# Performance work log

Hardware: AMD Instinct MI355X
Metric: run time of the kernel (lower is better)

The kernel has to match this reference:

```python
import jax, jax.numpy as jnp
import numpy as np

N, E, B = 128000, 512000, 128

def _conv1d(x, w, b):
    # x: [B,C,L], w: [O,I,K] (torch layout) -> valid conv, stride 1
    y = jax.lax.conv_general_dilated(x, w, (1,), 'VALID',
                                     dimension_numbers=('NCH', 'OIH', 'NCH'))
    return y + b[None, :, None]

def setup_inputs():
    key = jax.random.key(0)
    ks = jax.random.split(key, 22)
    def u(k, shape, fan_in):
        bound = 1.0 / np.sqrt(fan_in)
        return jax.random.uniform(k, shape, jnp.float32, -bound, bound)
    x = jax.random.normal(ks[0], (N, 33), jnp.float32)
    edge_index = jax.random.randint(ks[1], (2, E), 0, N, dtype=jnp.int64)
    batch = (jnp.arange(N, dtype=jnp.int64) * B) // N  # sorted, every graph non-empty
    target = jax.random.normal(ks[2], (B, 26, 1000), jnp.float32)
    return {
        'x': x, 'edge_index': edge_index, 'batch': batch, 'target': target,
        'lin_w': u(ks[3], (256, 33), 33), 'lin_b': jnp.zeros((256,), jnp.float32),
        'conv1_w': u(ks[4], (64, 26, 3), 26 * 3), 'conv1_b': u(ks[5], (64,), 26 * 3),
        'conv2_w': u(ks[6], (256, 64, 3), 64 * 3), 'conv2_b': u(ks[7], (256,), 64 * 3),
        'conv3_w': u(ks[8], (1024, 256, 5), 256 * 5), 'conv3_b': u(ks[9], (1024,), 256 * 5),
        'fc_w': u(ks[10], (768, 1024), 1024), 'fc_b': u(ks[11], (768,), 1024),
        'm1_w': u(ks[12], (1024, 1024), 1024), 'm1_b': u(ks[13], (1024,), 1024),
        'm2_w': u(ks[14], (1024, 1024), 1024), 'm2_b': u(ks[15], (1024,), 1024),
        'm3_w': u(ks[16], (512, 1024), 1024), 'm3_b': u(ks[17], (512,), 1024),
        'm4_w': u(ks[18], (1, 512), 512), 'm4_b': u(ks[19], (1,), 512),
    }

def reference(x, edge_index, batch, target,
              lin_w, lin_b, conv1_w, conv1_b, conv2_w, conv2_b,
              conv3_w, conv3_b, fc_w, fc_b,
              m1_w, m1_b, m2_w, m2_b, m3_w, m3_b, m4_w, m4_b):
    # ---- drug branch: GCN-normalized message passing, sum-aggr, graph mean ----
    xw = x @ lin_w.T                                   # [N,256]
    row, col = edge_index[0], edge_index[1]            # source j, target i
    deg = jax.ops.segment_sum(jnp.ones((E,), x.dtype), col, num_segments=N)
    dis = jnp.where(deg > 0, deg ** -0.5, 0.0)
    norm = dis[row] * dis[col]                         # [E]
    agg = jax.ops.segment_sum(norm[:, None] * xw[row], col, num_segments=N)
    out = agg + lin_b                                  # [N,256]
    sums = jax.ops.segment_sum(out, batch, num_segments=B)
    cnt = jax.ops.segment_sum(jnp.ones((N,), x.dtype), batch, num_segments=B)
    drug = jnp.where(cnt[:, None] > 0, sums / cnt[:, None], 0.0)  # [B,256]
    # ---- target branch: CNN (dropout = identity in eval) ----
    h = jax.nn.relu(_conv1d(target, conv1_w, conv1_b))
    h = jax.nn.relu(_conv1d(h, conv2_w, conv2_b))
    h = jax.nn.relu(_conv1d(h, conv3_w, conv3_b))
    h = jnp.max(h, axis=2)                             # AdaptiveMaxPool1d(1) -> [B,1024]
    tgt = jax.nn.relu(h @ fc_w.T + fc_b)               # [B,768]
    # ---- head MLP ----
    z = jnp.concatenate([drug, tgt], axis=1)           # [B,1024]
    z = jax.nn.relu(z @ m1_w.T + m1_b)
    z = jax.nn.relu(z @ m2_w.T + m2_b)
    z = jax.nn.relu(z @ m3_w.T + m3_b)
    return z @ m4_w.T + m4_b                           # [B,1]
```

## Files before the change

kernel.cpp:

```cpp
#include <hip/hip_runtime.h>

typedef unsigned short u16;
typedef __attribute__((ext_vector_type(8))) short short8;
typedef __attribute__((ext_vector_type(4))) float f32x4;

#define NN 128000
#define EE 512000
#define GB 128

#define GLDS16(g, l)                                                     \
  __builtin_amdgcn_global_load_lds(                                      \
      (const __attribute__((address_space(1))) unsigned int*)(g),        \
      (__attribute__((address_space(3))) unsigned int*)(l), 16, 0, 0)

__device__ __forceinline__ float u2f(u16 u) {
  union { unsigned u32; float f; } v; v.u32 = ((unsigned)u) << 16; return v.f;
}
__device__ __forceinline__ u16 f2bf(float x) {
  union { float f; unsigned u; } v; v.f = x;
  unsigned r = v.u + 0x7FFF + ((v.u >> 16) & 1);
  return (u16)(r >> 16);
}

__global__ void k_transpose(const float* lin_w, const float* w1, const float* w2, const float* w3,
                            float* lin_wT, float* w1T, u16* w2t, u16* w3r) {
  int idx = blockIdx.x * 256 + threadIdx.x;
  if (idx < 8448) { int i = idx >> 8, o = idx & 255; lin_wT[idx] = lin_w[o * 33 + i]; return; }
  idx -= 8448;
  if (idx < 4992) { int o = idx & 63, ck = idx >> 6; w1T[idx] = w1[o * 78 + ck]; return; }
  idx -= 4992;
  if (idx < 49152) {
    int c = idx & 63, o = (idx >> 6) & 255, k = idx >> 14;
    w2t[idx] = f2bf(w2[o * 192 + c * 3 + k]);
    return;
  }
  idx -= 49152;
  if (idx < 1310720) {
    int k    = idx >> 18;
    int r    = idx & 262143;
    int ot   = r >> 16;
    int wn   = (r >> 14) & 3;
    int j    = (r >> 12) & 3;
    int cb   = (r >> 9) & 7;
    int quad = (r >> 7) & 3;
    int l16  = (r >> 3) & 15;
    int i    = r & 7;
    int o = ot * 256 + wn * 64 + j * 16 + l16;
    int c = cb * 32 + quad * 8 + i;
    w3r[idx] = f2bf(w3[o * 1280 + c * 5 + k]);
  }
}

__global__ void k_deg_start(const int* ei, const int* batch, int* deg, int* start, int* hist) {
  __shared__ int lh[GB];
  int tid = threadIdx.x, blk = blockIdx.x;
  if (tid < GB) lh[tid] = 0;
  __syncthreads();
  int e0 = blk * 1024;
#pragma unroll
  for (int t = 0; t < 4; t++) {
    int e = e0 + t * 256 + tid;
    int col = ei[EE + e];
    atomicAdd(&deg[col], 1);
    atomicAdd(&lh[batch[col]], 1);
  }
  int i = blk * 256 + tid;
  int b = batch[i];
  if (i == 0) start[0] = 0;
  else if (b != batch[i - 1]) start[b] = i;
  if (i == NN - 1) start[GB] = NN;
  __syncthreads();
  if (tid < GB && lh[tid]) atomicAdd(&hist[tid * 16], lh[tid]);
}

__global__ void k_prefix(const int* hist, int* off, int* cursor) {
  __shared__ int h[GB];
  int tid = threadIdx.x;
  h[tid] = hist[tid * 16];
  __syncthreads();
  int s = 0;
  for (int j = 0; j < tid; j++) s += h[j];
  off[tid] = s;
  cursor[tid * 16] = s;
  if (tid == GB - 1) off[GB] = s + h[GB - 1];
}

__global__ void k_xw(const float* x, const float* lin_wT, const int* deg, u16* xw, float* dis) {
  __shared__ float xs[32][34];
  int tid = threadIdx.x, n0 = blockIdx.x * 32;
  int q = tid >> 6, lane = tid & 63;
  for (int n = q; n < 32; n += 4)
    if (lane < 33) xs[n][lane] = x[(n0 + n) * 33 + lane];
  float w[33];
#pragma unroll
  for (int i = 0; i < 33; i++) w[i] = lin_wT[i * 256 + tid];
  __syncthreads();
  for (int n = 0; n < 32; n++) {
    float acc = 0.f;
#pragma unroll
    for (int i = 0; i < 33; i++) acc += w[i] * xs[n][i];
    xw[(size_t)(n0 + n) * 256 + tid] = f2bf(acc);
  }
  if (tid < 32) { int d = deg[n0 + tid]; dis[n0 + tid] = d > 0 ? rsqrtf((float)d) : 0.f; }
}

__global__ void k_scatter(const int* ei, const int* batch, const float* dis,
                          int* cursor, uint2* bucket) {
  __shared__ int lh[GB];
  __shared__ int lbase[GB];
  int tid = threadIdx.x, blk = blockIdx.x;
  if (tid < GB) lh[tid] = 0;
  __syncthreads();
  int e0 = blk * 1024;
  int row[4], g[4], rk[4]; float nrm[4];
#pragma unroll
  for (int t = 0; t < 4; t++) {
    int e = e0 + t * 256 + tid;
    int r = ei[e], c = ei[EE + e];
    row[t] = r;
    g[t] = batch[c];
    nrm[t] = dis[r] * dis[c];
    rk[t] = atomicAdd(&lh[g[t]], 1);
  }
  __syncthreads();
  if (tid < GB && lh[tid]) lbase[tid] = atomicAdd(&cursor[tid * 16], lh[tid]);
  __syncthreads();
#pragma unroll
  for (int t = 0; t < 4; t++) {
    uint2 v; v.x = (unsigned)row[t]; v.y = __float_as_uint(nrm[t]);
    bucket[lbase[g[t]] + rk[t]] = v;
  }
}

__global__ void k_gather(const uint2* bucket, const int* off, const u16* xw, float* gsum) {
  __shared__ float red[4][256];
  int tid = threadIdx.x;
  int s = blockIdx.x, g = blockIdx.y;
  int lo = off[g], hi = off[g + 1];
  int cnt = hi - lo;
  int per = (cnt + 15) >> 4;
  int b0 = lo + s * per, b1 = min(b0 + per, hi);
  int lane = tid & 63, wid = tid >> 6;
  f32x4 acc = {0.f, 0.f, 0.f, 0.f};
  const u16* xbase = xw + lane * 4;
#pragma unroll 8
  for (int e = b0 + wid; e < b1; e += 4) {
    uint2 be = bucket[e];
    float nrm = __uint_as_float(be.y);
    ushort4 v = *(const ushort4*)(xbase + (size_t)be.x * 256);
    acc.x = fmaf(nrm, u2f(v.x), acc.x);
    acc.y = fmaf(nrm, u2f(v.y), acc.y);
    acc.z = fmaf(nrm, u2f(v.z), acc.z);
    acc.w = fmaf(nrm, u2f(v.w), acc.w);
  }
  *(f32x4*)&red[wid][lane * 4] = acc;
  __syncthreads();
  float v = red[0][tid] + red[1][tid] + red[2][tid] + red[3][tid];
  if (v != 0.f) atomicAdd(&gsum[tid * 128 + g], v);
}

__global__ void k_conv1(const float* target, const float* w1T, const float* b1, u16* h1T) {
  __shared__ float ts[26][132];
  __shared__ float wls[78 * 64];
  int tid = threadIdx.x, lt = blockIdx.x, bl = blockIdx.y;
  int l0 = lt * 128;
  int q = tid >> 6, lane = tid & 63;
  for (int c = q; c < 26; c += 4)
    for (int i = lane; i < 130; i += 64)
      ts[c][i] = target[(bl * 26 + c) * 1000 + min(l0 + i, 999)];
  for (int i = tid; i < 4992; i += 256) wls[i] = w1T[i];
  __syncthreads();
  int o = tid & 63, wid = tid >> 6;
  float w[78];
#pragma unroll
  for (int i = 0; i < 78; i++) w[i] = wls[i * 64 + o];
  float bias = b1[o];
  for (int t = 0; t < 32; t++) {
    int li = wid * 32 + t;
    float acc = bias;
#pragma unroll
    for (int c = 0; c < 26; c++)
#pragma unroll
      for (int k = 0; k < 3; k++) acc += ts[c][li + k] * w[c * 3 + k];
    int lg = l0 + li;
    if (lg < 998) h1T[((size_t)bl * 1000 + lg) * 64 + o] = f2bf(fmaxf(acc, 0.f));
  }
}

__global__ void k_conv2(const u16* h1T, const u16* w2t, const float* b2, u16* h2T) {
  __shared__ __align__(16) u16 als[132 * 32];
  __shared__ __align__(16) u16 bls[3 * 128 * 32];
  int tid = threadIdx.x;
  int lt = blockIdx.x, ot = blockIdx.y, bl = blockIdx.z;
  int l0 = lt * 128, o0 = ot * 128;
  int lane = tid & 63, wid = tid >> 6;
  int wm = wid >> 1, wn = wid & 1;
  int quad = lane >> 4, l16 = lane & 15;
  const f32x4 zero = {0.f, 0.f, 0.f, 0.f};
  f32x4 acc[4][4];
#pragma unroll
  for (int i = 0; i < 4; i++)
#pragma unroll
    for (int j = 0; j < 4; j++) acc[i][j] = zero;
  for (int cb = 0; cb < 2; cb++) {
    int c0 = cb * 32;
#pragma unroll
    for (int rr = 0; rr < 2; rr++) {
      int cid = rr * 256 + wid * 64 + lane;
      int row = cid >> 2, ch = (cid & 3) ^ (row & 3);
      GLDS16(h1T + ((size_t)bl * 1000 + min(l0 + row, 997)) * 64 + c0 + ch * 8,
             als + (rr * 256 + wid * 64) * 8);
    }
    if (wid == 0 && lane < 8) {
      int cid = 512 + lane;
      int row = cid >> 2, ch = (cid & 3) ^ (row & 3);
      GLDS16(h1T + ((size_t)bl * 1000 + min(l0 + row, 997)) * 64 + c0 + ch * 8, als + 512 * 8);
    }
#pragma unroll
    for (int rr = 0; rr < 6; rr++) {
      int cid = rr * 256 + wid * 64 + lane;
      int rko = cid >> 2, k = rko >> 7, o = rko & 127;
      int ch = (cid & 3) ^ (rko & 3);
      GLDS16(w2t + ((size_t)(k * 256 + o0 + o)) * 64 + c0 + ch * 8,
             bls + (rr * 256 + wid * 64) * 8);
    }
    __syncthreads();
#pragma unroll
    for (int k = 0; k < 3; k++) {
      short8 af[4], bfr[4];
#pragma unroll
      for (int i = 0; i < 4; i++) {
        int row = k + wm * 64 + i * 16 + l16;
        af[i] = *(const short8*)(als + row * 32 + ((quad ^ (row & 3)) * 8));
      }
#pragma unroll
      for (int j = 0; j < 4; j++) {
        int rowB = wn * 64 + j * 16 + l16;
        bfr[j] = *(const short8*)(bls + (k * 128 + rowB) * 32 + ((quad ^ (rowB & 3)) * 8));
      }
#pragma unroll
      for (int i = 0; i < 4; i++)
#pragma unroll
        for (int j = 0; j < 4; j++)
          acc[i][j] = __builtin_amdgcn_mfma_f32_16x16x32_bf16(af[i], bfr[j], acc[i][j], 0, 0, 0);
    }
    __syncthreads();
  }
#pragma unroll
  for (int j = 0; j < 4; j++) {
    int col = o0 + wn * 64 + j * 16 + l16;
    float bias = b2[col];
#pragma unroll
    for (int i = 0; i < 4; i++)
#pragma unroll
      for (int r = 0; r < 4; r++) {
        int lg = l0 + wm * 64 + i * 16 + quad * 4 + r;
        if (lg < 996)
          h2T[((size_t)bl * 996 + lg) * 256 + col] = f2bf(fmaxf(acc[i][j][r] + bias, 0.f));
      }
  }
}

__global__ void __launch_bounds__(256, 2)
k_conv3(const u16* h2T, const u16* w3r, const float* b3, float* pooledT) {
  __shared__ __align__(16) u16 als[136 * 128];
  __shared__ float mbuf[256];
  int bid = blockIdx.x;
  int xc = bid & 7, rr0 = bid >> 3;
  int ot = rr0 & 3, bl = xc * 16 + (rr0 >> 2);
  int o0 = ot * 256;
  int tid = threadIdx.x;
  int lane = tid & 63, wn = tid >> 6;
  int quad = lane >> 4, l16 = lane & 15;
  float omax[4];
#pragma unroll
  for (int j = 0; j < 4; j++) omax[j] = -3.0e38f;
  const f32x4 zero = {0.f, 0.f, 0.f, 0.f};
  const u16* wbase = w3r + ((size_t)(ot * 4 + wn)) * 16384 + lane * 8;
  for (int lt = 0; lt < 8; lt++) {
    int l0 = lt * 128;
    f32x4 acc[8][4];
#pragma unroll
    for (int i = 0; i < 8; i++)
#pragma unroll
      for (int j = 0; j < 4; j++) acc[i][j] = zero;
#pragma unroll 1
    for (int st = 0; st < 2; st++) {
#pragma unroll
      for (int rr = 0; rr < 8; rr++) {
        int cid = rr * 256 + tid;
        int row = cid >> 4, pp = cid & 15;
        int cc = (pp - row) & 15;
        GLDS16(h2T + ((size_t)bl * 996 + min(l0 + row, 995)) * 256 + st * 128 + cc * 8,
               als + (rr * 256 + wn * 64) * 8);
      }
      if (wn < 2) {
        int cid = 2048 + wn * 64 + lane;
        int row = cid >> 4, pp = cid & 15;
        int cc = (pp - row) & 15;
        GLDS16(h2T + ((size_t)bl * 996 + min(l0 + row, 995)) * 256 + st * 128 + cc * 8,
               als + (2048 + wn * 64) * 8);
      }
      __syncthreads();
#pragma unroll 1
      for (int cb = 0; cb < 4; cb++) {
#pragma unroll
        for (int k = 0; k < 5; k++) {
          short8 breg[4];
#pragma unroll
          for (int j = 0; j < 4; j++)
            breg[j] = *(const short8*)(wbase + (size_t)k * 262144 + (size_t)j * 4096 +
                                       (size_t)(st * 4 + cb) * 512);
#pragma unroll
          for (int i = 0; i < 8; i++) {
            int row = k + i * 16 + l16;
            int pp = (cb * 4 + quad + row) & 15;
            short8 af = *(const short8*)(als + row * 128 + pp * 8);
#pragma unroll
            for (int j = 0; j < 4; j++)
              acc[i][j] = __builtin_amdgcn_mfma_f32_16x16x32_bf16(af, breg[j], acc[i][j],
                                                                  0, 0, 0);
          }
        }
      }
      __syncthreads();
    }
#pragma unroll
    for (int i = 0; i < 8; i++) {
#pragma unroll
      for (int r = 0; r < 4; r++) {
        int lg = l0 + i * 16 + quad * 4 + r;
        if (lg < 992) {
#pragma unroll
          for (int j = 0; j < 4; j++) omax[j] = fmaxf(omax[j], acc[i][j][r]);
        }
      }
    }
  }
#pragma unroll
  for (int j = 0; j < 4; j++) {
    omax[j] = fmaxf(omax[j], __shfl_xor(omax[j], 16, 64));
    omax[j] = fmaxf(omax[j], __shfl_xor(omax[j], 32, 64));
  }
  if (quad == 0) {
#pragma unroll
    for (int j = 0; j < 4; j++) mbuf[wn * 64 + j * 16 + l16] = omax[j];
  }
  __syncthreads();
  {
    float v = mbuf[tid] + b3[o0 + tid];
    pooledT[(size_t)(o0 + tid) * 128 + bl] = fmaxf(v, 0.f);
  }
}

__global__ void k_z0(const float* gsum, const int* start, const float* lin_b, const float* tgtT,
                     float* z0T) {
  int idx = blockIdx.x * 256 + threadIdx.x;
  int r = idx >> 7, bb = idx & 127;
  float v;
  if (r < 256) {
    float c = (float)(start[bb + 1] - start[bb]);
    v = gsum[idx] / c + lin_b[r];
  } else {
    v = tgtT[(r - 256) * 128 + bb];
  }
  z0T[idx] = v;
}

__global__ void k_fc4(const float* zT, const float* W, const float* bias, float* outT,
                      int K, int O) {
  __shared__ float wls[4 * 1024];
  int tid = threadIdx.x;
  int o0 = blockIdx.x * 4;
  for (int idx = tid; idx < 4 * K; idx += 512) {
    int oo = idx / K, i = idx - oo * K;
    wls[oo * K + i] = W[(size_t)(o0 + oo) * K + i];
  }
  __syncthreads();
  int osub = tid >> 7, bb = tid & 127;
  int o = o0 + osub;
  float acc = 0.f;
  const float* wp = &wls[osub * K];
#pragma unroll 8
  for (int i = 0; i < K; i++) acc = fmaf(wp[i], zT[i * 128 + bb], acc);
  acc += bias[o];
  outT[(size_t)o * 128 + bb] = fmaxf(acc, 0.f);
}

__global__ void k_fc_final(const float* zT, const float* W, const float* bias, float* final_out,
                           int K) {
  __shared__ float wls[512];
  int tid = threadIdx.x;
  for (int i = tid; i < K; i += 256) wls[i] = W[i];
  __syncthreads();
  if (tid >= 128) return;
  int bb = tid;
  float acc = 0.f;
#pragma unroll 8
  for (int i = 0; i < K; i++) acc = fmaf(wls[i], zT[i * 128 + bb], acc);
  final_out[bb] = acc + bias[0];
}

extern "C" void kernel_launch(void* const* d_in, const int* in_sizes, int n_in,
                              void* d_out, int out_size, void* d_ws, size_t ws_size,
                              hipStream_t stream) {
  const float* x      = (const float*)d_in[0];
  const int*   ei     = (const int*)d_in[1];
  const int*   batch  = (const int*)d_in[2];
  const float* target = (const float*)d_in[3];
  const float* lin_w  = (const float*)d_in[4];
  const float* lin_b  = (const float*)d_in[5];
  const float* w1     = (const float*)d_in[6];
  const float* b1     = (const float*)d_in[7];
  const float* w2     = (const float*)d_in[8];
  const float* b2     = (const float*)d_in[9];
  const float* w3     = (const float*)d_in[10];
  const float* b3     = (const float*)d_in[11];
  const float* fcw    = (const float*)d_in[12];
  const float* fcb    = (const float*)d_in[13];
  const float* m1w = (const float*)d_in[14]; const float* m1b = (const float*)d_in[15];
  const float* m2w = (const float*)d_in[16]; const float* m2b = (const float*)d_in[17];
  const float* m3w = (const float*)d_in[18]; const float* m3b = (const float*)d_in[19];
  const float* m4w = (const float*)d_in[20]; const float* m4b = (const float*)d_in[21];

  char* ws = (char*)d_ws;
  size_t ofs = 0;
  auto alloc = [&](size_t bytes) -> void* {
    void* p = ws + ofs;
    ofs = (ofs + bytes + 255) & ~(size_t)255;
    return p;
  };
  int*   deg    = (int*)alloc((size_t)NN * 4);
  float* dis    = (float*)alloc((size_t)NN * 4);
  int*   start  = (int*)alloc((size_t)(GB + 1) * 4);
  int*   hist   = (int*)alloc((size_t)GB * 16 * 4);
  int*   off    = (int*)alloc((size_t)(GB + 1) * 4);
  int*   cursor = (int*)alloc((size_t)GB * 16 * 4);
  uint2* bucket = (uint2*)alloc((size_t)EE * 8);
  float* gsum   = (float*)alloc((size_t)256 * 128 * 4);
  float* lin_wT = (float*)alloc((size_t)33 * 256 * 4);
  float* w1T    = (float*)alloc((size_t)78 * 64 * 4);
  u16*   w2t    = (u16*)alloc((size_t)3 * 256 * 64 * 2);
  u16*   w3r    = (u16*)alloc((size_t)5 * 1024 * 256 * 2);
  float* pooledT= (float*)alloc((size_t)1024 * 128 * 4);
  float* tgtT   = (float*)alloc((size_t)768 * 128 * 4);
  float* z0T    = (float*)alloc((size_t)1024 * 128 * 4);
  float* z1T    = (float*)alloc((size_t)1024 * 128 * 4);
  float* z2T    = (float*)alloc((size_t)1024 * 128 * 4);
  float* z3T    = (float*)alloc((size_t)512 * 128 * 4);
  size_t F_end = ofs;

  u16* xw  = (u16*)(ws + F_end);
  u16* h1T = (u16*)(ws + F_end);
  u16* h2T = (u16*)(ws + F_end + (size_t)128 * 1000 * 64 * 2);

  hipMemsetAsync(deg, 0, (size_t)NN * 4, stream);
  hipMemsetAsync(hist, 0, (size_t)GB * 16 * 4, stream);
  hipMemsetAsync(gsum, 0, (size_t)256 * 128 * 4, stream);

  k_transpose<<<5365, 256, 0, stream>>>(lin_w, w1, w2, w3, lin_wT, w1T, w2t, w3r);
  k_deg_start<<<500, 256, 0, stream>>>(ei, batch, deg, start, hist);
  k_prefix<<<1, 128, 0, stream>>>(hist, off, cursor);
  k_xw<<<4000, 256, 0, stream>>>(x, lin_wT, deg, xw, dis);
  k_scatter<<<500, 256, 0, stream>>>(ei, batch, dis, cursor, bucket);
  k_gather<<<dim3(16, GB), 256, 0, stream>>>(bucket, off, xw, gsum);

  k_conv1<<<dim3(8, 128), 256, 0, stream>>>(target, w1T, b1, h1T);
  k_conv2<<<dim3(8, 2, 128), 256, 0, stream>>>(h1T, w2t, b2, h2T);
  k_conv3<<<512, 256, 0, stream>>>(h2T, w3r, b3, pooledT);

  k_fc4<<<192, 512, 0, stream>>>(pooledT, fcw, fcb, tgtT, 1024, 768);
  k_z0<<<512, 256, 0, stream>>>(gsum, start, lin_b, tgtT, z0T);
  k_fc4<<<256, 512, 0, stream>>>(z0T, m1w, m1b, z1T, 1024, 1024);
  k_fc4<<<256, 512, 0, stream>>>(z1T, m2w, m2b, z2T, 1024, 1024);
  k_fc4<<<128, 512, 0, stream>>>(z2T, m3w, m3b, z3T, 1024, 512);
  k_fc_final<<<1, 256, 0, stream>>>(z3T, m4w, m4b, (float*)d_out, 512);
}
```

Measured before the change: 841.3 us.

## Repack conv3 weights by step and double-buffer B-fragment loads in registers

Reorders the bf16 conv3 weight packing so each (st, cb, k) step's B fragments for a wave sit in one contiguous 32K-element slab. The conv3 inner loop is unrolled into explicit steps that prefetch the next step's weight fragments into a second register set while the current set feeds the MFMAs, wrapping back to step 0 across l-tiles. The aim is to hide global weight-load latency behind matrix math. It costs extra VGPRs under the two-blocks-per-CU launch bound, which may cause spills or lower occupancy.

Result: slower. 1.100 ms (+30.8%).

```diff
diff --git a/kernel.cpp b/kernel.cpp
--- a/kernel.cpp
+++ b/kernel.cpp
@@ -23,7 +23,7 @@
 }
 
 __global__ void k_transpose(const float* lin_w, const float* w1, const float* w2, const float* w3,
-                            float* lin_wT, float* w1T, u16* w2t, u16* w3r) {
+                            float* lin_wT, float* w1T, u16* w2t, u16* w3p) {
   int idx = blockIdx.x * 256 + threadIdx.x;
   if (idx < 8448) { int i = idx >> 8, o = idx & 255; lin_wT[idx] = lin_w[o * 33 + i]; return; }
   idx -= 8448;
@@ -36,18 +36,14 @@
   }
   idx -= 49152;
   if (idx < 1310720) {
-    int k    = idx >> 18;
-    int r    = idx & 262143;
-    int ot   = r >> 16;
-    int wn   = (r >> 14) & 3;
-    int j    = (r >> 12) & 3;
-    int cb   = (r >> 9) & 7;
-    int quad = (r >> 7) & 3;
-    int l16  = (r >> 3) & 15;
-    int i    = r & 7;
-    int o = ot * 256 + wn * 64 + j * 16 + l16;
-    int c = cb * 32 + quad * 8 + i;
-    w3r[idx] = f2bf(w3[o * 1280 + c * 5 + k]);
+    int stcbk = idx >> 15;
+    int fi    = (idx >> 9) & 63;
+    int r512  = idx & 511;
+    int quad  = r512 >> 7, l16 = (r512 >> 3) & 15, i = r512 & 7;
+    int stcb  = stcbk / 5, k = stcbk - stcb * 5;
+    int o = fi * 16 + l16;
+    int c = stcb * 32 + quad * 8 + i;
+    w3p[idx] = f2bf(w3[o * 1280 + c * 5 + k]);
   }
 }
 
@@ -261,8 +257,32 @@
   }
 }
 
+#define LOADB(dst, s)                                                          \
+  do {                                                                         \
+    const u16* p_ = wb + (size_t)(s) * 32768;                                  \
+    dst[0] = *(const short8*)(p_);                                             \
+    dst[1] = *(const short8*)(p_ + 512);                                       \
+    dst[2] = *(const short8*)(p_ + 1024);                                      \
+    dst[3] = *(const short8*)(p_ + 1536);                                      \
+  } while (0)
+
+#define STEP(CUR, NXT, KK, CBV, SNEXT)                                         \
+  do {                                                                         \
+    LOADB(NXT, SNEXT);                                                         \
+    _Pragma("unroll")                                                          \
+    for (int i = 0; i < 8; i++) {                                              \
+      int row = (KK) + i * 16 + l16;                                           \
+      int pp = ((CBV) * 4 + quad + row) & 15;                                  \
+      short8 af = *(const short8*)(als + row * 128 + pp * 8);                  \
+      acc[i][0] = __builtin_amdgcn_mfma_f32_16x16x32_bf16(af, CUR[0], acc[i][0], 0, 0, 0); \
+      acc[i][1] = __builtin_amdgcn_mfma_f32_16x16x32_bf16(af, CUR[1], acc[i][1], 0, 0, 0); \
+      acc[i][2] = __builtin_amdgcn_mfma_f32_16x16x32_bf16(af, CUR[2], acc[i][2], 0, 0, 0); \
+      acc[i][3] = __builtin_amdgcn_mfma_f32_16x16x32_bf16(af, CUR[3], acc[i][3], 0, 0, 0); \
+    }                                                                          \
+  } while (0)
+
 __global__ void __launch_bounds__(256, 2)
-k_conv3(const u16* h2T, const u16* w3r, const float* b3, float* pooledT) {
+k_conv3(const u16* h2T, const u16* w3p, const float* b3, float* pooledT) {
   __shared__ __align__(16) u16 als[136 * 128];
   __shared__ float mbuf[256];
   int bid = blockIdx.x;
@@ -276,7 +296,9 @@
 #pragma unroll
   for (int j = 0; j < 4; j++) omax[j] = -3.0e38f;
   const f32x4 zero = {0.f, 0.f, 0.f, 0.f};
-  const u16* wbase = w3r + ((size_t)(ot * 4 + wn)) * 16384 + lane * 8;
+  const u16* wb = w3p + (size_t)(ot * 16 + wn * 4) * 512 + lane * 8;
+  short8 bA[4], bB[4];
+  LOADB(bA, 0);
   for (int lt = 0; lt < 8; lt++) {
     int l0 = lt * 128;
     f32x4 acc[8][4];
@@ -303,25 +325,20 @@
       }
       __syncthreads();
 #pragma unroll 1
-      for (int cb = 0; cb < 4; cb++) {
-#pragma unroll
-        for (int k = 0; k < 5; k++) {
-          short8 breg[4];
-#pragma unroll
-          for (int j = 0; j < 4; j++)
-            breg[j] = *(const short8*)(wbase + (size_t)k * 262144 + (size_t)j * 4096 +
-                                       (size_t)(st * 4 + cb) * 512);
-#pragma unroll
-          for (int i = 0; i < 8; i++) {
-            int row = k + i * 16 + l16;
-            int pp = (cb * 4 + quad + row) & 15;
-            short8 af = *(const short8*)(als + row * 128 + pp * 8);
-#pragma unroll
-            for (int j = 0; j < 4; j++)
-              acc[i][j] = __builtin_amdgcn_mfma_f32_16x16x32_bf16(af, breg[j], acc[i][j],
-                                                                  0, 0, 0);
-          }
-        }
+      for (int cbp = 0; cbp < 2; cbp++) {
+        int cb0 = cbp * 2, cb1 = cb0 + 1;
+        int sb = st * 20 + cbp * 10;
+        int swrap = (sb == 30) ? 0 : sb + 10;
+        STEP(bA, bB, 0, cb0, sb + 1);
+        STEP(bB, bA, 1, cb0, sb + 2);
+        STEP(bA, bB, 2, cb0, sb + 3);
+        STEP(bB, bA, 3, cb0, sb + 4);
+        STEP(bA, bB, 4, cb0, sb + 5);
+        STEP(bB, bA, 0, cb1, sb + 6);
+        STEP(bA, bB, 1, cb1, sb + 7);
+        STEP(bB, bA, 2, cb1, sb + 8);
+        STEP(bA, bB, 3, cb1, sb + 9);
+        STEP(bB, bA, 4, cb1, swrap);
       }
       __syncthreads();
     }
@@ -441,7 +458,7 @@
   float* lin_wT = (float*)alloc((size_t)33 * 256 * 4);
   float* w1T    = (float*)alloc((size_t)78 * 64 * 4);
   u16*   w2t    = (u16*)alloc((size_t)3 * 256 * 64 * 2);
-  u16*   w3r    = (u16*)alloc((size_t)5 * 1024 * 256 * 2);
+  u16*   w3p    = (u16*)alloc((size_t)5 * 1024 * 256 * 2);
   float* pooledT= (float*)alloc((size_t)1024 * 128 * 4);
   float* tgtT   = (float*)alloc((size_t)768 * 128 * 4);
   float* z0T    = (float*)alloc((size_t)1024 * 128 * 4);
@@ -458,7 +475,7 @@
   hipMemsetAsync(hist, 0, (size_t)GB * 16 * 4, stream);
   hipMemsetAsync(gsum, 0, (size_t)256 * 128 * 4, stream);
 
-  k_transpose<<<5365, 256, 0, stream>>>(lin_w, w1, w2, w3, lin_wT, w1T, w2t, w3r);
+  k_transpose<<<5365, 256, 0, stream>>>(lin_w, w1, w2, w3, lin_wT, w1T, w2t, w3p);
   k_deg_start<<<500, 256, 0, stream>>>(ei, batch, deg, start, hist);
   k_prefix<<<1, 128, 0, stream>>>(hist, off, cursor);
   k_xw<<<4000, 256, 0, stream>>>(x, lin_wT, deg, xw, dis);
@@ -467,7 +484,7 @@
 
   k_conv1<<<dim3(8, 128), 256, 0, stream>>>(target, w1T, b1, h1T);
   k_conv2<<<dim3(8, 2, 128), 256, 0, stream>>>(h1T, w2t, b2, h2T);
-  k_conv3<<<512, 256, 0, stream>>>(h2T, w3r, b3, pooledT);
+  k_conv3<<<512, 256, 0, stream>>>(h2T, w3p, b3, pooledT);
 
   k_fc4<<<192, 512, 0, stream>>>(pooledT, fcw, fcb, tgtT, 1024, 768);
   k_z0<<<512, 256, 0, stream>>>(gsum, start, lin_b, tgtT, z0T);
```

## Warp-specialize conv3 with dedicated loader wave and double-buffered LDS

Applied to the files above, without the earlier changes.

Adds a fifth wavefront to the conv3 block that only streams h2T tiles into two alternating LDS buffers via global_load_lds. The four compute waves wait on a single barrier per phase, replacing the load-then-syncthreads pattern twice per phase, so input loads overlap MFMA work. The conv3 weights are repacked so each (stage, channel block, tap) slice is contiguous, which simplifies the B-fragment addressing. In exchange LDS per block doubles and the launch bound drops its min-blocks hint, which may lower occupancy, and correctness depends on the producer and consumers issuing matching barrier counts.

After: 880.7 us. +4.7%, slower.

```diff
diff --git a/kernel.cpp b/kernel.cpp
--- a/kernel.cpp
+++ b/kernel.cpp
@@ -23,7 +23,7 @@
 }
 
 __global__ void k_transpose(const float* lin_w, const float* w1, const float* w2, const float* w3,
-                            float* lin_wT, float* w1T, u16* w2t, u16* w3r) {
+                            float* lin_wT, float* w1T, u16* w2t, u16* w3p) {
   int idx = blockIdx.x * 256 + threadIdx.x;
   if (idx < 8448) { int i = idx >> 8, o = idx & 255; lin_wT[idx] = lin_w[o * 33 + i]; return; }
   idx -= 8448;
@@ -36,18 +36,14 @@
   }
   idx -= 49152;
   if (idx < 1310720) {
-    int k    = idx >> 18;
-    int r    = idx & 262143;
-    int ot   = r >> 16;
-    int wn   = (r >> 14) & 3;
-    int j    = (r >> 12) & 3;
-    int cb   = (r >> 9) & 7;
-    int quad = (r >> 7) & 3;
-    int l16  = (r >> 3) & 15;
-    int i    = r & 7;
-    int o = ot * 256 + wn * 64 + j * 16 + l16;
-    int c = cb * 32 + quad * 8 + i;
-    w3r[idx] = f2bf(w3[o * 1280 + c * 5 + k]);
+    int stcbk = idx >> 15;
+    int fi    = (idx >> 9) & 63;
+    int r512  = idx & 511;
+    int quad  = r512 >> 7, l16 = (r512 >> 3) & 15, i = r512 & 7;
+    int stcb  = stcbk / 5, k = stcbk - stcb * 5;
+    int o = fi * 16 + l16;
+    int c = stcb * 32 + quad * 8 + i;
+    w3p[idx] = f2bf(w3[o * 1280 + c * 5 + k]);
   }
 }
 
@@ -261,24 +257,44 @@
   }
 }
 
-__global__ void __launch_bounds__(256, 2)
-k_conv3(const u16* h2T, const u16* w3r, const float* b3, float* pooledT) {
-  __shared__ __align__(16) u16 als[136 * 128];
+__global__ void __launch_bounds__(320)
+k_conv3(const u16* h2T, const u16* w3p, const float* b3, float* pooledT) {
+  __shared__ __align__(16) u16 als[2][2176 * 8];
   __shared__ float mbuf[256];
   int bid = blockIdx.x;
   int xc = bid & 7, rr0 = bid >> 3;
   int ot = rr0 & 3, bl = xc * 16 + (rr0 >> 2);
   int o0 = ot * 256;
   int tid = threadIdx.x;
-  int lane = tid & 63, wn = tid >> 6;
+  int lane = tid & 63, wid = tid >> 6;
+
+  if (wid == 4) {
+    for (int ph = 0; ph < 16; ph++) {
+      int lt = ph >> 1, st = ph & 1, l0 = lt * 128;
+      u16* dst = als[st];
+#pragma unroll
+      for (int c = 0; c < 34; c++) {
+        int cid = c * 64 + lane;
+        int row = cid >> 4, pp = cid & 15;
+        int cc = (pp - row) & 15;
+        GLDS16(h2T + ((size_t)bl * 996 + min(l0 + row, 995)) * 256 + st * 128 + cc * 8,
+               dst + cid * 8);
+      }
+      asm volatile("s_waitcnt vmcnt(0)" ::: "memory");
+      __builtin_amdgcn_s_barrier();
+    }
+    __syncthreads();
+    return;
+  }
+
+  int wn = wid;
   int quad = lane >> 4, l16 = lane & 15;
   float omax[4];
 #pragma unroll
   for (int j = 0; j < 4; j++) omax[j] = -3.0e38f;
   const f32x4 zero = {0.f, 0.f, 0.f, 0.f};
-  const u16* wbase = w3r + ((size_t)(ot * 4 + wn)) * 16384 + lane * 8;
+  const u16* wb = w3p + (size_t)(ot * 16 + wn * 4) * 512 + lane * 8;
   for (int lt = 0; lt < 8; lt++) {
-    int l0 = lt * 128;
     f32x4 acc[8][4];
 #pragma unroll
     for (int i = 0; i < 8; i++)
@@ -286,45 +302,32 @@
       for (int j = 0; j < 4; j++) acc[i][j] = zero;
 #pragma unroll 1
     for (int st = 0; st < 2; st++) {
-#pragma unroll
-      for (int rr = 0; rr < 8; rr++) {
-        int cid = rr * 256 + tid;
-        int row = cid >> 4, pp = cid & 15;
-        int cc = (pp - row) & 15;
-        GLDS16(h2T + ((size_t)bl * 996 + min(l0 + row, 995)) * 256 + st * 128 + cc * 8,
-               als + (rr * 256 + wn * 64) * 8);
-      }
-      if (wn < 2) {
-        int cid = 2048 + wn * 64 + lane;
-        int row = cid >> 4, pp = cid & 15;
-        int cc = (pp - row) & 15;
-        GLDS16(h2T + ((size_t)bl * 996 + min(l0 + row, 995)) * 256 + st * 128 + cc * 8,
-               als + (2048 + wn * 64) * 8);
-      }
-      __syncthreads();
+      __builtin_amdgcn_s_barrier();
+      const u16* a = als[st];
 #pragma unroll 1
       for (int cb = 0; cb < 4; cb++) {
 #pragma unroll
         for (int k = 0; k < 5; k++) {
+          const u16* p_ = wb + (size_t)(st * 20 + cb * 5 + k) * 32768;
           short8 breg[4];
-#pragma unroll
-          for (int j = 0; j < 4; j++)
-            breg[j] = *(const short8*)(wbase + (size_t)k * 262144 + (size_t)j * 4096 +
-                                       (size_t)(st * 4 + cb) * 512);
+          breg[0] = *(const short8*)(p_);
+          breg[1] = *(const short8*)(p_ + 512);
+          breg[2] = *(const short8*)(p_ + 1024);
+          breg[3] = *(const short8*)(p_ + 1536);
 #pragma unroll
           for (int i = 0; i < 8; i++) {
             int row = k + i * 16 + l16;
             int pp = (cb * 4 + quad + row) & 15;
-            short8 af = *(const short8*)(als + row * 128 + pp * 8);
-#pragma unroll
-            for (int j = 0; j < 4; j++)
-              acc[i][j] = __builtin_amdgcn_mfma_f32_16x16x32_bf16(af, breg[j], acc[i][j],
-                                                                  0, 0, 0);
+            short8 af = *(const short8*)(a + row * 128 + pp * 8);
+            acc[i][0] = __builtin_amdgcn_mfma_f32_16x16x32_bf16(af, breg[0], acc[i][0], 0, 0, 0);
+            acc[i][1] = __builtin_amdgcn_mfma_f32_16x16x32_bf16(af, breg[1], acc[i][1], 0, 0, 0);
+            acc[i][2] = __builtin_amdgcn_mfma_f32_16x16x32_bf16(af, breg[2], acc[i][2], 0, 0, 0);
+            acc[i][3] = __builtin_amdgcn_mfma_f32_16x16x32_bf16(af, breg[3], acc[i][3], 0, 0, 0);
           }
         }
       }
-      __syncthreads();
-    }
+    }
+    int l0 = lt * 128;
 #pragma unroll
     for (int i = 0; i < 8; i++) {
 #pragma unroll
@@ -441,7 +444,7 @@
   float* lin_wT = (float*)alloc((size_t)33 * 256 * 4);
   float* w1T    = (float*)alloc((size_t)78 * 64 * 4);
   u16*   w2t    = (u16*)alloc((size_t)3 * 256 * 64 * 2);
-  u16*   w3r    = (u16*)alloc((size_t)5 * 1024 * 256 * 2);
+  u16*   w3p    = (u16*)alloc((size_t)5 * 1024 * 256 * 2);
   float* pooledT= (float*)alloc((size_t)1024 * 128 * 4);
   float* tgtT   = (float*)alloc((size_t)768 * 128 * 4);
   float* z0T    = (float*)alloc((size_t)1024 * 128 * 4);
@@ -458,7 +461,7 @@
   hipMemsetAsync(hist, 0, (size_t)GB * 16 * 4, stream);
   hipMemsetAsync(gsum, 0, (size_t)256 * 128 * 4, stream);
 
-  k_transpose<<<5365, 256, 0, stream>>>(lin_w, w1, w2, w3, lin_wT, w1T, w2t, w3r);
+  k_transpose<<<5365, 256, 0, stream>>>(lin_w, w1, w2, w3, lin_wT, w1T, w2t, w3p);
   k_deg_start<<<500, 256, 0, stream>>>(ei, batch, deg, start, hist);
   k_prefix<<<1, 128, 0, stream>>>(hist, off, cursor);
   k_xw<<<4000, 256, 0, stream>>>(x, lin_wT, deg, xw, dis);
@@ -467,7 +470,7 @@
 
   k_conv1<<<dim3(8, 128), 256, 0, stream>>>(target, w1T, b1, h1T);
   k_conv2<<<dim3(8, 2, 128), 256, 0, stream>>>(h1T, w2t, b2, h2T);
-  k_conv3<<<512, 256, 0, stream>>>(h2T, w3r, b3, pooledT);
+  k_conv3<<<512, 320, 0, stream>>>(h2T, w3p, b3, pooledT);
 
   k_fc4<<<192, 512, 0, stream>>>(pooledT, fcw, fcb, tgtT, 1024, 768);
   k_z0<<<512, 256, 0, stream>>>(gsum, start, lin_b, tgtT, z0T);
```
